# Kernel optimization log

Hardware: AMD Instinct MI355X
Metric: run time of the kernel (lower is better)

## Reference

```python
import jax, jax.numpy as jnp
import numpy as np
import math

HIDDEN = 768
HEADS = 12
HEAD_DIM = HIDDEN // HEADS  # 64
SEQ = 197
K_RANK = min(128, HEAD_DIM)  # 64
BATCH = 64


def setup_inputs() -> dict:
    key = jax.random.key(0)
    ks = jax.random.split(key, 12)
    init = 0.02
    # Linear weights stored [in, out] (equivalent to torch W.T)
    return {
        "hidden_states": jax.random.normal(ks[0], (BATCH, SEQ, HIDDEN), dtype=jnp.float32),
        "Wq": jax.random.normal(ks[1], (HIDDEN, HIDDEN), dtype=jnp.float32) * init,
        "bq": jnp.zeros((HIDDEN,), dtype=jnp.float32),
        "Wk": jax.random.normal(ks[2], (HIDDEN, HIDDEN), dtype=jnp.float32) * init,
        "bk": jnp.zeros((HIDDEN,), dtype=jnp.float32),
        "Wv": jax.random.normal(ks[3], (HIDDEN, HIDDEN), dtype=jnp.float32) * init,
        "bv": jnp.zeros((HIDDEN,), dtype=jnp.float32),
        "Wo": jax.random.normal(ks[4], (HIDDEN, HIDDEN), dtype=jnp.float32) * init,
        "bo": jnp.zeros((HIDDEN,), dtype=jnp.float32),
        "E_k": jax.random.normal(ks[5], (SEQ, K_RANK), dtype=jnp.float32) * init,
        "E_v": jax.random.normal(ks[6], (SEQ, K_RANK), dtype=jnp.float32) * init,
    }


def reference(hidden_states, Wq, bq, Wk, bk, Wv, bv, Wo, bo, E_k, E_v):
    B, S, D = hidden_states.shape
    H, d = HEADS, HEAD_DIM
    scale = 1.0 / math.sqrt(d)

    def split_heads(x):  # [B,S,D] -> [B,H,S,d]
        return x.reshape(B, S, H, d).transpose(0, 2, 1, 3)

    q = split_heads(hidden_states @ Wq + bq)
    k = split_heads(hidden_states @ Wk + bk)
    v = split_heads(hidden_states @ Wv + bv)

    # low-rank projection of K/V along the sequence axis: [B,H,k,d]
    pk = jnp.einsum('sk,bhsd->bhkd', E_k, k)
    pv = jnp.einsum('sk,bhsd->bhkd', E_v, v)

    # scores over reduced axis: [B,H,S,k]
    scores = jnp.einsum('bhsd,bhkd->bhsk', q, pk) * scale
    probs = jax.nn.softmax(scores, axis=-1)

    ctx = jnp.einsum('bhsk,bhkd->bhsd', probs, pv)
    ctx = ctx.transpose(0, 2, 1, 3).reshape(B, S, D)
    out = ctx @ Wo + bo  # dropout rate 0.0 -> identity
    return out
```

## Files before the change

kernel.cpp:

```cpp
#include <hip/hip_runtime.h>
#include <math.h>

#define B_   64
#define S_   197
#define D_   768
#define H_   12
#define HD_  64
#define M_   (B_ * S_)
#define MPAD 12672
#define KE   224
#define BH_  (B_ * H_)
#define WSZ  ((size_t)D_ * D_)

typedef _Float16 half8_t __attribute__((ext_vector_type(8)));
typedef _Float16 half4_t __attribute__((ext_vector_type(4)));
typedef _Float16 half2_t __attribute__((ext_vector_type(2)));
typedef float floatx4 __attribute__((ext_vector_type(4)));

#define LDS_DMA16(gptr, lptr) \
  __builtin_amdgcn_global_load_lds((const __attribute__((address_space(1))) void*)(gptr), \
                                   (__attribute__((address_space(3))) void*)(lptr), 16, 0, 0)

__global__ __launch_bounds__(256) void prep_kernel(
    const float* __restrict__ X,
    const float* __restrict__ Wq, const float* __restrict__ Wk,
    const float* __restrict__ Wv, const float* __restrict__ Wo,
    const float* __restrict__ Ek, const float* __restrict__ Ev,
    _Float16* __restrict__ Xh,
    _Float16* __restrict__ Tcat, _Float16* __restrict__ To,
    _Float16* __restrict__ EET,
    float* __restrict__ esumK, float* __restrict__ esumV)
{
    __shared__ float tile[32][33];
    const int bid = blockIdx.x, tid = threadIdx.x;
    if (bid < 9504) {
        const int i4 = (bid * 256 + tid) * 4;
        float4 v = make_float4(0.f, 0.f, 0.f, 0.f);
        if (i4 < M_ * D_) v = *(const float4*)&X[i4];
        half4_t o = { (_Float16)v.x, (_Float16)v.y, (_Float16)v.z, (_Float16)v.w };
        *(half4_t*)&Xh[i4] = o;
        return;
    }
    int b2 = bid - 9504;
    if (b2 < 2304) {
        const int z = b2 / 576, rem = b2 % 576;
        const int bx = rem % 24, by = rem / 24;
        const float* W = (z == 0) ? Wk : (z == 1) ? Wv : (z == 2) ? Wq : Wo;
        _Float16* T = (z < 3) ? (Tcat + (size_t)z * WSZ) : To;
        const int n0 = bx * 32, k0 = by * 32;
        const int r = tid >> 3, c4 = (tid & 7) * 4;
        *(float4*)&tile[r][c4] = *(const float4*)&W[(size_t)(k0 + r) * D_ + n0 + c4];
        __syncthreads();
        half4_t o = { (_Float16)tile[c4 + 0][r], (_Float16)tile[c4 + 1][r],
                      (_Float16)tile[c4 + 2][r], (_Float16)tile[c4 + 3][r] };
        *(half4_t*)&T[(size_t)(n0 + r) * D_ + k0 + c4] = o;
        return;
    }
    b2 -= 2304;
    const float* E = b2 ? Ev : Ek;
    _Float16* ET = EET + (size_t)b2 * 64 * KE;
    float* es = b2 ? esumV : esumK;
    for (int i = tid; i < 64 * KE; i += 256) {
        const int rr = i / KE, s = i % KE;
        ET[i] = (_Float16)((s < S_) ? E[s * 64 + rr] : 0.f);
    }
    if (tid < 64) {
        float acc = 0.f;
        for (int s = 0; s < S_; ++s) acc += E[s * 64 + tid];
        es[tid] = acc;
    }
}

__global__ __launch_bounds__(256) void y_kernel(
    const _Float16* __restrict__ Xh, const _Float16* __restrict__ EET,
    _Float16* __restrict__ Ybuf)
{
    __shared__ _Float16 Xs[KE * 66];
    const int bid = blockIdx.x;
    const int b = bid / 12, n0 = (bid % 12) * 64;
    const int tid = threadIdx.x, w = tid >> 6, lane = tid & 63;
    const int l15 = lane & 15, quad = lane >> 4;

    #pragma unroll
    for (int i = 0; i < 7; ++i) {
        const int s = i * 32 + (tid >> 3);
        const int d0 = (tid & 7) * 8;
        const half8_t v = *(const half8_t*)&Xh[(size_t)(b * S_ + s) * D_ + n0 + d0];
        #pragma unroll
        for (int jj = 0; jj < 4; ++jj) {
            half2_t t2 = { v[2 * jj], v[2 * jj + 1] };
            *(half2_t*)&Xs[s * 66 + d0 + 2 * jj] = t2;
        }
    }
    __syncthreads();

    floatx4 acc[2][4] = {};
    #pragma unroll
    for (int k7 = 0; k7 < 7; ++k7) {
        half8_t af[2];
        #pragma unroll
        for (int mi = 0; mi < 2; ++mi)
            af[mi] = *(const half8_t*)&EET[(w * 32 + mi * 16 + l15) * KE + k7 * 32 + quad * 8];
        #pragma unroll
        for (int ni = 0; ni < 4; ++ni) {
            const int sb = k7 * 32 + quad * 8;
            half8_t bf;
            #pragma unroll
            for (int jj = 0; jj < 8; ++jj) bf[jj] = Xs[(sb + jj) * 66 + ni * 16 + l15];
            #pragma unroll
            for (int mi = 0; mi < 2; ++mi)
                acc[mi][ni] = __builtin_amdgcn_mfma_f32_16x16x32_f16(
                    af[mi], bf, acc[mi][ni], 0, 0, 0);
        }
    }

    #pragma unroll
    for (int mi = 0; mi < 2; ++mi)
        #pragma unroll
        for (int ni = 0; ni < 4; ++ni)
            #pragma unroll
            for (int i = 0; i < 4; ++i) {
                const int m_local = w * 32 + mi * 16 + quad * 4 + i;
                const int row = (m_local >> 6) * 4096 + b * 64 + (m_local & 63);
                Ybuf[(size_t)row * D_ + n0 + ni * 16 + l15] = (_Float16)acc[mi][ni][i];
            }
}


__global__ __launch_bounds__(256) void gemm_qpkv(
    const _Float16* __restrict__ Xh, const _Float16* __restrict__ Ybuf,
    const _Float16* __restrict__ Tcat,
    const float* __restrict__ bq, const float* __restrict__ bk,
    const float* __restrict__ bv,
    const float* __restrict__ esumK, const float* __restrict__ esumV,
    _Float16* __restrict__ Qh, _Float16* __restrict__ pk16,
    _Float16* __restrict__ pvT)
{
    __shared__ _Float16 sm[16384];
    const int bid = blockIdx.x;
    const _Float16 *A, *W;
    const float *bias, *esum;
    _Float16* O16;
    bool pvmode = false;
    int m0, n0;
    if (bid < 624) {
        const int xcd = bid & 7, t = bid >> 3;
        const int slot = t / 6, j = t - slot * 6;
        const int m_blk = slot * 8 + xcd;
        if (m_blk >= MPAD / 128) return;
        m0 = m_blk * 128; n0 = j * 128;
        A = Xh; W = Tcat + 2 * WSZ + (size_t)n0 * D_;
        bias = bq; esum = nullptr; O16 = Qh;
    } else {
        const int b2 = bid - 624;
        const int xcd = b2 & 7, t = b2 >> 3;
        const int slot = t / 6, j = t - slot * 6;
        const int m_blk = slot * 8 + xcd;
        m0 = m_blk * 128; n0 = j * 128;
        pvmode = (m_blk >= 32);
        A = Ybuf; W = Tcat + (pvmode ? WSZ : 0) + (size_t)n0 * D_;
        bias = pvmode ? bv : bk; esum = pvmode ? esumV : esumK;
        O16 = pk16;
    }

    const int tid = threadIdx.x;
    const int w = tid >> 6, lane = tid & 63;
    const int fr = lane & 15, quad = lane >> 4, f7 = lane & 7;
    const int l3 = lane >> 3;
    const int csrc = ((lane & 7) ^ l3) * 8;
    const int wm = (w >> 1) * 64, wn = (w & 1) * 64;

    const _Float16* Abase = A + (size_t)(m0 + w * 32 + l3) * D_ + csrc;
    const _Float16* Wbase = W + (size_t)(w * 32 + l3) * D_ + csrc;

    floatx4 acc[4][4] = {};

    for (int k0 = 0; k0 < D_; k0 += 64) {
        #pragma unroll
        for (int j = 0; j < 4; ++j) {
            LDS_DMA16(Abase + (size_t)(j * 8) * D_ + k0, &sm[w * 2048 + j * 512]);
            LDS_DMA16(Wbase + (size_t)(j * 8) * D_ + k0, &sm[8192 + w * 2048 + j * 512]);
        }
        __syncthreads();
        #pragma unroll
        for (int ksub = 0; ksub < 2; ++ksub) {
            const int sa = ((ksub * 4 + quad) ^ f7) * 8;
            half8_t af[4], bf[4];
            #pragma unroll
            for (int i = 0; i < 4; ++i) {
                af[i] = *(const half8_t*)&sm[(wm + i * 16 + fr) * 64 + sa];
                bf[i] = *(const half8_t*)&sm[8192 + (wn + i * 16 + fr) * 64 + sa];
            }
            #pragma unroll
            for (int mi = 0; mi < 4; ++mi)
                #pragma unroll
                for (int ni = 0; ni < 4; ++ni)
                    acc[mi][ni] = __builtin_amdgcn_mfma_f32_16x16x32_f16(
                        af[mi], bf[ni], acc[mi][ni], 0, 0, 0);
        }
        __syncthreads();
    }

    float bval[4];
    #pragma unroll
    for (int ni = 0; ni < 4; ++ni)
        bval[ni] = bias[n0 + wn + ni * 16 + fr];

    if (pvmode) {
        const int bb = (m0 - 4096 + wm) >> 6;
        #pragma unroll
        for (int mi = 0; mi < 4; ++mi) {
            const float4 es4 = *(const float4*)&esum[mi * 16 + quad * 4];
            const float esv[4] = {es4.x, es4.y, es4.z, es4.w};
            #pragma unroll
            for (int ni = 0; ni < 4; ++ni) {
                const int n = n0 + wn + ni * 16 + fr;
                const int h = n >> 6, d = n & 63;
                #pragma unroll
                for (int i = 0; i < 4; ++i) {
                    const int r = mi * 16 + quad * 4 + i;
                    pvT[((size_t)(bb * H_ + h)) * 4096 + d * 64 + r] =
                        (_Float16)(acc[mi][ni][i] + esv[i] * bval[ni]);
                }
            }
        }
    } else {
        _Float16* ct = &sm[w * 2176];
        #pragma unroll
        for (int half = 0; half < 2; ++half) {
            #pragma unroll
            for (int mi2 = 0; mi2 < 2; ++mi2) {
                const int mi = half * 2 + mi2;
                float esv[4] = {1.f, 1.f, 1.f, 1.f};
                if (esum) {
                    const float4 es4 = *(const float4*)&esum[mi * 16 + quad * 4];
                    esv[0] = es4.x; esv[1] = es4.y; esv[2] = es4.z; esv[3] = es4.w;
                }
                #pragma unroll
                for (int ni = 0; ni < 4; ++ni)
                    #pragma unroll
                    for (int i = 0; i < 4; ++i)
                        ct[(mi2 * 16 + quad * 4 + i) * 68 + ni * 16 + fr] =
                            (_Float16)(acc[mi][ni][i] + esv[i] * bval[ni]);
            }
            #pragma unroll
            for (int pass = 0; pass < 4; ++pass) {
                const int rr = pass * 8 + (lane >> 3);
                const int cc = (lane & 7) * 8;
                const half8_t v = *(const half8_t*)&ct[rr * 68 + cc];
                *(half8_t*)&O16[(size_t)(m0 + wm + half * 32 + rr) * D_ + n0 + wn + cc] = v;
            }
        }
    }
}

__global__ __launch_bounds__(256) void gemm_o(
    const _Float16* __restrict__ CTX, const _Float16* __restrict__ To,
    const float* __restrict__ bo, float* __restrict__ O32)
{
    __shared__ _Float16 sm[16384];
    const int xcd = blockIdx.x & 7, t = blockIdx.x >> 3;
    const int slot = t / 6, j = t - slot * 6;
    const int m_blk = slot * 8 + xcd;
    if (m_blk >= MPAD / 128) return;
    const int m0 = m_blk * 128, n0 = j * 128;

    const int tid = threadIdx.x;
    const int w = tid >> 6, lane = tid & 63;
    const int fr = lane & 15, quad = lane >> 4, f7 = lane & 7;
    const int l3 = lane >> 3;
    const int csrc = ((lane & 7) ^ l3) * 8;
    const int wm = (w >> 1) * 64, wn = (w & 1) * 64;

    const _Float16* Abase = CTX + (size_t)(m0 + w * 32 + l3) * D_ + csrc;
    const _Float16* Wbase = To + (size_t)(n0 + w * 32 + l3) * D_ + csrc;

    floatx4 acc[4][4] = {};

    for (int k0 = 0; k0 < D_; k0 += 64) {
        #pragma unroll
        for (int j2 = 0; j2 < 4; ++j2) {
            LDS_DMA16(Abase + (size_t)(j2 * 8) * D_ + k0, &sm[w * 2048 + j2 * 512]);
            LDS_DMA16(Wbase + (size_t)(j2 * 8) * D_ + k0, &sm[8192 + w * 2048 + j2 * 512]);
        }
        __syncthreads();
        #pragma unroll
        for (int ksub = 0; ksub < 2; ++ksub) {
            const int sa = ((ksub * 4 + quad) ^ f7) * 8;
            half8_t af[4], bf[4];
            #pragma unroll
            for (int i = 0; i < 4; ++i) {
                af[i] = *(const half8_t*)&sm[(wm + i * 16 + fr) * 64 + sa];
                bf[i] = *(const half8_t*)&sm[8192 + (wn + i * 16 + fr) * 64 + sa];
            }
            #pragma unroll
            for (int mi = 0; mi < 4; ++mi)
                #pragma unroll
                for (int ni = 0; ni < 4; ++ni)
                    acc[mi][ni] = __builtin_amdgcn_mfma_f32_16x16x32_f16(
                        af[mi], bf[ni], acc[mi][ni], 0, 0, 0);
        }
        __syncthreads();
    }

    float bval[4];
    #pragma unroll
    for (int ni = 0; ni < 4; ++ni)
        bval[ni] = bo[n0 + wn + ni * 16 + fr];

    const int rq = quad * 4;
    if (m0 + 128 <= M_) {
        #pragma unroll
        for (int ni = 0; ni < 4; ++ni) {
            const int n = n0 + wn + ni * 16 + fr;
            #pragma unroll
            for (int mi = 0; mi < 4; ++mi)
                #pragma unroll
                for (int i = 0; i < 4; ++i)
                    O32[(size_t)(m0 + wm + mi * 16 + rq + i) * D_ + n] =
                        acc[mi][ni][i] + bval[ni];
        }
    } else {
        #pragma unroll
        for (int ni = 0; ni < 4; ++ni) {
            const int n = n0 + wn + ni * 16 + fr;
            #pragma unroll
            for (int mi = 0; mi < 4; ++mi)
                #pragma unroll
                for (int i = 0; i < 4; ++i) {
                    const int m = m0 + wm + mi * 16 + rq + i;
                    if (m < M_)
                        O32[(size_t)m * D_ + n] = acc[mi][ni][i] + bval[ni];
                }
        }
    }
}

__global__ __launch_bounds__(256) void attn_kernel(
    const _Float16* __restrict__ Qh, const _Float16* __restrict__ pk16,
    const _Float16* __restrict__ pvT, _Float16* __restrict__ CTXh)
{
    __shared__ _Float16 P[64 * 80];
    const int bh = blockIdx.x, b = bh / H_, h = bh % H_;
    const int tid = threadIdx.x, w = tid >> 6, lane = tid & 63;
    const int l15 = lane & 15, quad = lane >> 4;
    const _Float16* pkB = pk16 + (size_t)(b * 64) * D_ + h * 64;
    const _Float16* pvB = pvT + (size_t)bh * 4096;
    const size_t qbase = (size_t)(b * S_) * D_ + h * HD_;

    half8_t bkf[4][2], bvf[4][2];
    #pragma unroll
    for (int ni = 0; ni < 4; ++ni)
        #pragma unroll
        for (int kk = 0; kk < 2; ++kk) {
            bkf[ni][kk] = *(const half8_t*)&pkB[(size_t)(ni * 16 + l15) * D_ + kk * 32 + quad * 8];
            bvf[ni][kk] = *(const half8_t*)&pvB[(ni * 16 + l15) * 64 + kk * 32 + quad * 8];
        }

    for (int t = w; t < 13; t += 4) {
        const int srow = t * 16;
        floatx4 acc[4] = {};
        #pragma unroll
        for (int kk = 0; kk < 2; ++kk) {
            const half8_t aq = *(const half8_t*)
                &Qh[qbase + (size_t)(srow + l15) * D_ + kk * 32 + quad * 8];
            #pragma unroll
            for (int ni = 0; ni < 4; ++ni)
                acc[ni] = __builtin_amdgcn_mfma_f32_16x16x32_f16(
                    aq, bkf[ni][kk], acc[ni], 0, 0, 0);
        }
        float p[4][4];
        #pragma unroll
        for (int i = 0; i < 4; ++i) {
            const float s0 = acc[0][i] * 0.125f, s1 = acc[1][i] * 0.125f;
            const float s2 = acc[2][i] * 0.125f, s3 = acc[3][i] * 0.125f;
            float mx = fmaxf(fmaxf(s0, s1), fmaxf(s2, s3));
            #pragma unroll
            for (int off = 1; off < 16; off <<= 1)
                mx = fmaxf(mx, __shfl_xor(mx, off, 64));
            const float e0 = __expf(s0 - mx), e1 = __expf(s1 - mx);
            const float e2 = __expf(s2 - mx), e3 = __expf(s3 - mx);
            float sme = e0 + e1 + e2 + e3;
            #pragma unroll
            for (int off = 1; off < 16; off <<= 1)
                sme += __shfl_xor(sme, off, 64);
            const float inv = 1.f / sme;
            p[0][i] = e0 * inv; p[1][i] = e1 * inv;
            p[2][i] = e2 * inv; p[3][i] = e3 * inv;
        }
        #pragma unroll
        for (int ni = 0; ni < 4; ++ni)
            #pragma unroll
            for (int i = 0; i < 4; ++i)
                P[(w * 16 + quad * 4 + i) * 80 + ni * 16 + l15] = (_Float16)p[ni][i];

        floatx4 accv[4] = {};
        #pragma unroll
        for (int kk = 0; kk < 2; ++kk) {
            const half8_t ap = *(const half8_t*)&P[(w * 16 + l15) * 80 + kk * 32 + quad * 8];
            #pragma unroll
            for (int ni = 0; ni < 4; ++ni)
                accv[ni] = __builtin_amdgcn_mfma_f32_16x16x32_f16(
                    ap, bvf[ni][kk], accv[ni], 0, 0, 0);
        }
        #pragma unroll
        for (int ni = 0; ni < 4; ++ni)
            #pragma unroll
            for (int i = 0; i < 4; ++i) {
                const int s = srow + quad * 4 + i;
                if (s < S_)
                    CTXh[qbase + (size_t)s * D_ + ni * 16 + l15] = (_Float16)accv[ni][i];
            }
    }
}

extern "C" void kernel_launch(void* const* d_in, const int* in_sizes, int n_in,
                              void* d_out, int out_size, void* d_ws, size_t ws_size,
                              hipStream_t stream) {
    const float* X   = (const float*)d_in[0];
    const float* Wq  = (const float*)d_in[1];
    const float* bq  = (const float*)d_in[2];
    const float* Wk  = (const float*)d_in[3];
    const float* bk  = (const float*)d_in[4];
    const float* Wv  = (const float*)d_in[5];
    const float* bv  = (const float*)d_in[6];
    const float* Wo  = (const float*)d_in[7];
    const float* bo  = (const float*)d_in[8];
    const float* E_k = (const float*)d_in[9];
    const float* E_v = (const float*)d_in[10];
    float* out = (float*)d_out;

    char* p = (char*)d_ws;
    _Float16* Xh   = (_Float16*)p; p += (size_t)MPAD * D_ * 2;
    _Float16* Tcat = (_Float16*)p; p += (size_t)3 * WSZ * 2;
    _Float16* To   = (_Float16*)p; p += (size_t)WSZ * 2;
    _Float16* Qh   = (_Float16*)p; p += (size_t)MPAD * D_ * 2;
    _Float16* EET  = (_Float16*)p; p += (size_t)128 * KE * 2;
    float* esumK   = (float*)p;    p += 64 * sizeof(float);
    float* esumV   = (float*)p;    p += 64 * sizeof(float);
    _Float16* Ybuf = (_Float16*)p; p += (size_t)8192 * D_ * 2;
    _Float16* pk16 = (_Float16*)p; p += (size_t)4096 * D_ * 2;
    _Float16* pvT  = (_Float16*)p;

    prep_kernel<<<11810, 256, 0, stream>>>(X, Wq, Wk, Wv, Wo, E_k, E_v,
                                           Xh, Tcat, To, EET, esumK, esumV);
    y_kernel<<<768, 256, 0, stream>>>(Xh, EET, Ybuf);
    gemm_qpkv<<<1008, 256, 0, stream>>>(Xh, Ybuf, Tcat,
                                        bq, bk, bv, esumK, esumV,
                                        Qh, pk16, pvT);
    attn_kernel<<<BH_, 256, 0, stream>>>(Qh, pk16, pvT, Xh);
    gemm_o<<<624, 256, 0, stream>>>(Xh, To, bo, out);
}
```

Before: 218.9 us.

## Store pv row-major via LDS staging and halve gemm_o M-tile

```diff
diff --git a/kernel.cpp b/kernel.cpp
--- a/kernel.cpp
+++ b/kernel.cpp
@@ -126,7 +126,6 @@
             }
 }
 
-
 __global__ __launch_bounds__(256) void gemm_qpkv(
     const _Float16* __restrict__ Xh, const _Float16* __restrict__ Ybuf,
     const _Float16* __restrict__ Tcat,
@@ -134,21 +133,20 @@
     const float* __restrict__ bv,
     const float* __restrict__ esumK, const float* __restrict__ esumV,
     _Float16* __restrict__ Qh, _Float16* __restrict__ pk16,
-    _Float16* __restrict__ pvT)
+    _Float16* __restrict__ pv16)
 {
     __shared__ _Float16 sm[16384];
     const int bid = blockIdx.x;
     const _Float16 *A, *W;
     const float *bias, *esum;
     _Float16* O16;
-    bool pvmode = false;
-    int m0, n0;
+    int m0, n0, rowb;
     if (bid < 624) {
         const int xcd = bid & 7, t = bid >> 3;
         const int slot = t / 6, j = t - slot * 6;
         const int m_blk = slot * 8 + xcd;
         if (m_blk >= MPAD / 128) return;
-        m0 = m_blk * 128; n0 = j * 128;
+        m0 = m_blk * 128; n0 = j * 128; rowb = m0;
         A = Xh; W = Tcat + 2 * WSZ + (size_t)n0 * D_;
         bias = bq; esum = nullptr; O16 = Qh;
     } else {
@@ -157,10 +155,11 @@
         const int slot = t / 6, j = t - slot * 6;
         const int m_blk = slot * 8 + xcd;
         m0 = m_blk * 128; n0 = j * 128;
-        pvmode = (m_blk >= 32);
-        A = Ybuf; W = Tcat + (pvmode ? WSZ : 0) + (size_t)n0 * D_;
-        bias = pvmode ? bv : bk; esum = pvmode ? esumV : esumK;
-        O16 = pk16;
+        const bool pv = (m_blk >= 32);
+        rowb = pv ? m0 - 4096 : m0;
+        A = Ybuf; W = Tcat + (pv ? WSZ : 0) + (size_t)n0 * D_;
+        bias = pv ? bv : bk; esum = pv ? esumV : esumK;
+        O16 = pv ? pv16 : pk16;
     }
 
     const int tid = threadIdx.x;
@@ -206,50 +205,30 @@
     for (int ni = 0; ni < 4; ++ni)
         bval[ni] = bias[n0 + wn + ni * 16 + fr];
 
-    if (pvmode) {
-        const int bb = (m0 - 4096 + wm) >> 6;
-        #pragma unroll
-        for (int mi = 0; mi < 4; ++mi) {
-            const float4 es4 = *(const float4*)&esum[mi * 16 + quad * 4];
-            const float esv[4] = {es4.x, es4.y, es4.z, es4.w};
-            #pragma unroll
-            for (int ni = 0; ni < 4; ++ni) {
-                const int n = n0 + wn + ni * 16 + fr;
-                const int h = n >> 6, d = n & 63;
+    _Float16* ct = &sm[w * 2176];
+    #pragma unroll
+    for (int half = 0; half < 2; ++half) {
+        #pragma unroll
+        for (int mi2 = 0; mi2 < 2; ++mi2) {
+            const int mi = half * 2 + mi2;
+            float esv[4] = {1.f, 1.f, 1.f, 1.f};
+            if (esum) {
+                const float4 es4 = *(const float4*)&esum[mi * 16 + quad * 4];
+                esv[0] = es4.x; esv[1] = es4.y; esv[2] = es4.z; esv[3] = es4.w;
+            }
+            #pragma unroll
+            for (int ni = 0; ni < 4; ++ni)
                 #pragma unroll
-                for (int i = 0; i < 4; ++i) {
-                    const int r = mi * 16 + quad * 4 + i;
-                    pvT[((size_t)(bb * H_ + h)) * 4096 + d * 64 + r] =
+                for (int i = 0; i < 4; ++i)
+                    ct[(mi2 * 16 + quad * 4 + i) * 68 + ni * 16 + fr] =
                         (_Float16)(acc[mi][ni][i] + esv[i] * bval[ni]);
-                }
-            }
-        }
-    } else {
-        _Float16* ct = &sm[w * 2176];
-        #pragma unroll
-        for (int half = 0; half < 2; ++half) {
-            #pragma unroll
-            for (int mi2 = 0; mi2 < 2; ++mi2) {
-                const int mi = half * 2 + mi2;
-                float esv[4] = {1.f, 1.f, 1.f, 1.f};
-                if (esum) {
-                    const float4 es4 = *(const float4*)&esum[mi * 16 + quad * 4];
-                    esv[0] = es4.x; esv[1] = es4.y; esv[2] = es4.z; esv[3] = es4.w;
-                }
-                #pragma unroll
-                for (int ni = 0; ni < 4; ++ni)
-                    #pragma unroll
-                    for (int i = 0; i < 4; ++i)
-                        ct[(mi2 * 16 + quad * 4 + i) * 68 + ni * 16 + fr] =
-                            (_Float16)(acc[mi][ni][i] + esv[i] * bval[ni]);
-            }
-            #pragma unroll
-            for (int pass = 0; pass < 4; ++pass) {
-                const int rr = pass * 8 + (lane >> 3);
-                const int cc = (lane & 7) * 8;
-                const half8_t v = *(const half8_t*)&ct[rr * 68 + cc];
-                *(half8_t*)&O16[(size_t)(m0 + wm + half * 32 + rr) * D_ + n0 + wn + cc] = v;
-            }
+        }
+        #pragma unroll
+        for (int pass = 0; pass < 4; ++pass) {
+            const int rr = pass * 8 + (lane >> 3);
+            const int cc = (lane & 7) * 8;
+            const half8_t v = *(const half8_t*)&ct[rr * 68 + cc];
+            *(half8_t*)&O16[(size_t)(rowb + wm + half * 32 + rr) * D_ + n0 + wn + cc] = v;
         }
     }
 }
@@ -258,43 +237,45 @@
     const _Float16* __restrict__ CTX, const _Float16* __restrict__ To,
     const float* __restrict__ bo, float* __restrict__ O32)
 {
-    __shared__ _Float16 sm[16384];
+    __shared__ _Float16 sm[12288];
     const int xcd = blockIdx.x & 7, t = blockIdx.x >> 3;
     const int slot = t / 6, j = t - slot * 6;
     const int m_blk = slot * 8 + xcd;
-    if (m_blk >= MPAD / 128) return;
-    const int m0 = m_blk * 128, n0 = j * 128;
+    if (m_blk >= MPAD / 64) return;
+    const int m0 = m_blk * 64, n0 = j * 128;
 
     const int tid = threadIdx.x;
     const int w = tid >> 6, lane = tid & 63;
     const int fr = lane & 15, quad = lane >> 4, f7 = lane & 7;
     const int l3 = lane >> 3;
     const int csrc = ((lane & 7) ^ l3) * 8;
-    const int wm = (w >> 1) * 64, wn = (w & 1) * 64;
-
-    const _Float16* Abase = CTX + (size_t)(m0 + w * 32 + l3) * D_ + csrc;
+    const int wm = (w >> 1) * 32, wn = (w & 1) * 64;
+
+    const _Float16* Abase = CTX + (size_t)(m0 + w * 16 + l3) * D_ + csrc;
     const _Float16* Wbase = To + (size_t)(n0 + w * 32 + l3) * D_ + csrc;
 
-    floatx4 acc[4][4] = {};
+    floatx4 acc[2][4] = {};
 
     for (int k0 = 0; k0 < D_; k0 += 64) {
         #pragma unroll
-        for (int j2 = 0; j2 < 4; ++j2) {
-            LDS_DMA16(Abase + (size_t)(j2 * 8) * D_ + k0, &sm[w * 2048 + j2 * 512]);
-            LDS_DMA16(Wbase + (size_t)(j2 * 8) * D_ + k0, &sm[8192 + w * 2048 + j2 * 512]);
-        }
+        for (int j2 = 0; j2 < 2; ++j2)
+            LDS_DMA16(Abase + (size_t)(j2 * 8) * D_ + k0, &sm[w * 1024 + j2 * 512]);
+        #pragma unroll
+        for (int j2 = 0; j2 < 4; ++j2)
+            LDS_DMA16(Wbase + (size_t)(j2 * 8) * D_ + k0, &sm[4096 + w * 2048 + j2 * 512]);
         __syncthreads();
         #pragma unroll
         for (int ksub = 0; ksub < 2; ++ksub) {
             const int sa = ((ksub * 4 + quad) ^ f7) * 8;
-            half8_t af[4], bf[4];
-            #pragma unroll
-            for (int i = 0; i < 4; ++i) {
+            half8_t af[2], bf[4];
+            #pragma unroll
+            for (int i = 0; i < 2; ++i)
                 af[i] = *(const half8_t*)&sm[(wm + i * 16 + fr) * 64 + sa];
-                bf[i] = *(const half8_t*)&sm[8192 + (wn + i * 16 + fr) * 64 + sa];
-            }
-            #pragma unroll
-            for (int mi = 0; mi < 4; ++mi)
+            #pragma unroll
+            for (int i = 0; i < 4; ++i)
+                bf[i] = *(const half8_t*)&sm[4096 + (wn + i * 16 + fr) * 64 + sa];
+            #pragma unroll
+            for (int mi = 0; mi < 2; ++mi)
                 #pragma unroll
                 for (int ni = 0; ni < 4; ++ni)
                     acc[mi][ni] = __builtin_amdgcn_mfma_f32_16x16x32_f16(
@@ -309,12 +290,12 @@
         bval[ni] = bo[n0 + wn + ni * 16 + fr];
 
     const int rq = quad * 4;
-    if (m0 + 128 <= M_) {
+    if (m0 + 64 <= M_) {
         #pragma unroll
         for (int ni = 0; ni < 4; ++ni) {
             const int n = n0 + wn + ni * 16 + fr;
             #pragma unroll
-            for (int mi = 0; mi < 4; ++mi)
+            for (int mi = 0; mi < 2; ++mi)
                 #pragma unroll
                 for (int i = 0; i < 4; ++i)
                     O32[(size_t)(m0 + wm + mi * 16 + rq + i) * D_ + n] =
@@ -325,7 +306,7 @@
         for (int ni = 0; ni < 4; ++ni) {
             const int n = n0 + wn + ni * 16 + fr;
             #pragma unroll
-            for (int mi = 0; mi < 4; ++mi)
+            for (int mi = 0; mi < 2; ++mi)
                 #pragma unroll
                 for (int i = 0; i < 4; ++i) {
                     const int m = m0 + wm + mi * 16 + rq + i;
@@ -338,14 +319,14 @@
 
 __global__ __launch_bounds__(256) void attn_kernel(
     const _Float16* __restrict__ Qh, const _Float16* __restrict__ pk16,
-    const _Float16* __restrict__ pvT, _Float16* __restrict__ CTXh)
+    const _Float16* __restrict__ pv16, _Float16* __restrict__ CTXh)
 {
     __shared__ _Float16 P[64 * 80];
     const int bh = blockIdx.x, b = bh / H_, h = bh % H_;
     const int tid = threadIdx.x, w = tid >> 6, lane = tid & 63;
     const int l15 = lane & 15, quad = lane >> 4;
     const _Float16* pkB = pk16 + (size_t)(b * 64) * D_ + h * 64;
-    const _Float16* pvB = pvT + (size_t)bh * 4096;
+    const _Float16* pvB = pv16 + (size_t)(b * 64) * D_ + h * 64;
     const size_t qbase = (size_t)(b * S_) * D_ + h * HD_;
 
     half8_t bkf[4][2], bvf[4][2];
@@ -354,7 +335,9 @@
         #pragma unroll
         for (int kk = 0; kk < 2; ++kk) {
             bkf[ni][kk] = *(const half8_t*)&pkB[(size_t)(ni * 16 + l15) * D_ + kk * 32 + quad * 8];
-            bvf[ni][kk] = *(const half8_t*)&pvB[(ni * 16 + l15) * 64 + kk * 32 + quad * 8];
+            #pragma unroll
+            for (int jj = 0; jj < 8; ++jj)
+                bvf[ni][kk][jj] = pvB[(size_t)(kk * 32 + quad * 8 + jj) * D_ + ni * 16 + l15];
         }
 
     for (int t = w; t < 13; t += 4) {
@@ -440,14 +423,14 @@
     float* esumV   = (float*)p;    p += 64 * sizeof(float);
     _Float16* Ybuf = (_Float16*)p; p += (size_t)8192 * D_ * 2;
     _Float16* pk16 = (_Float16*)p; p += (size_t)4096 * D_ * 2;
-    _Float16* pvT  = (_Float16*)p;
+    _Float16* pv16 = (_Float16*)p;
 
     prep_kernel<<<11810, 256, 0, stream>>>(X, Wq, Wk, Wv, Wo, E_k, E_v,
                                            Xh, Tcat, To, EET, esumK, esumV);
     y_kernel<<<768, 256, 0, stream>>>(Xh, EET, Ybuf);
     gemm_qpkv<<<1008, 256, 0, stream>>>(Xh, Ybuf, Tcat,
                                         bq, bk, bv, esumK, esumV,
-                                        Qh, pk16, pvT);
-    attn_kernel<<<BH_, 256, 0, stream>>>(Qh, pk16, pvT, Xh);
-    gemm_o<<<624, 256, 0, stream>>>(Xh, To, bo, out);
-}
+                                        Qh, pk16, pv16);
+    attn_kernel<<<BH_, 256, 0, stream>>>(Qh, pk16, pv16, Xh);
+    gemm_o<<<1200, 256, 0, stream>>>(Xh, To, bo, out);
+}
```

Result: faster. 210.8 us (-3.7%).
